# Kernel optimization log

Hardware: AMD Instinct MI355X
Metric: run time of the kernel (lower is better)

Reference implementation:

```python
import jax, jax.numpy as jnp
import numpy as np

DIM = 1024
NUM_HEADS = 16
HEAD_DIM = DIM // NUM_HEADS
B, S = 2, 2048


def setup_inputs() -> dict:
    key = jax.random.key(0)
    k1, k2, k3 = jax.random.split(key, 3)
    x = jax.random.normal(k1, (B, S, DIM), dtype=jnp.float32)
    # torch Linear stores weight [out,in]; we store transposed [in,out] for x @ W
    w_qkv = jax.random.normal(k2, (DIM, 3 * DIM), dtype=jnp.float32) * (DIM ** -0.5)
    b_qkv = jnp.zeros((3 * DIM,), dtype=jnp.float32)
    w_proj = jax.random.normal(k3, (DIM, DIM), dtype=jnp.float32) * (DIM ** -0.5)
    b_proj = jnp.zeros((DIM,), dtype=jnp.float32)
    return {"x": x, "w_qkv": w_qkv, "b_qkv": b_qkv, "w_proj": w_proj, "b_proj": b_proj}


def reference(x, w_qkv, b_qkv, w_proj, b_proj):
    b, s, d = x.shape
    h = HEAD_DIM
    qkv = x @ w_qkv + b_qkv                              # [b,s,3d]
    qkv = qkv.reshape(b, s, 3, NUM_HEADS, h)
    q = jnp.transpose(qkv[:, :, 0], (0, 2, 1, 3))        # [b,nh,s,h]
    k = jnp.transpose(qkv[:, :, 1], (0, 2, 1, 3))
    v = jnp.transpose(qkv[:, :, 2], (0, 2, 1, 3))
    scores = jnp.einsum("bnqh,bnkh->bnqk", q, k) * (h ** -0.5)  # [b,nh,s,s]
    attn = jax.nn.softmax(scores, axis=-1)               # attn_drop is identity (p=0)
    out = jnp.einsum("bnqk,bnkh->bnqh", attn, v)         # [b,nh,s,h]
    out = jnp.transpose(out, (0, 2, 1, 3)).reshape(b, s, d)
    out = out @ w_proj + b_proj                          # proj_drop is identity (p=0)
    return out
```

## Files before the change

### kernel.cpp

```cpp
#include <hip/hip_runtime.h>
#include <hip/hip_bf16.h>

#define DIM    1024
#define NHEADS 16
#define HDIM   64
#define BB     2
#define SS     2048
#define MTOT   (BB * SS)

typedef unsigned short u16;
typedef __attribute__((ext_vector_type(8))) short short8;
typedef __attribute__((ext_vector_type(4))) float f32x4;

__device__ inline u16 f2b(float f) {
  __hip_bfloat16 h = __float2bfloat16(f);
  return *reinterpret_cast<u16*>(&h);
}
__device__ inline f32x4 zero4() { f32x4 v = {0.f, 0.f, 0.f, 0.f}; return v; }

#define GLD_LDS16(GP, LP)                                                   \
  __builtin_amdgcn_global_load_lds(                                         \
      (const __attribute__((address_space(1))) unsigned int*)               \
          (unsigned long long)(const void*)(GP),                            \
      (__attribute__((address_space(3))) unsigned int*)                     \
          (unsigned int)(unsigned long long)(const void*)(LP),              \
      16, 0, 0)

#define QSCALE 0.18033688011112042f

__global__ __launch_bounds__(256) void prep_kernel(
    const float* __restrict__ x, const float* __restrict__ wq,
    const float* __restrict__ wp,
    u16* __restrict__ x_bf, u16* __restrict__ wqt, u16* __restrict__ wpt) {
  __shared__ u16 tile[32][36];
  const int t   = threadIdx.x;
  const int blk = blockIdx.x;
  if (blk < 2048) {
    const int i = blk * 256 + t;
    const float4 a = ((const float4*)x)[i * 2];
    const float4 b = ((const float4*)x)[i * 2 + 1];
    union { u16 u[8]; uint4 v; } r;
    r.u[0] = f2b(a.x); r.u[1] = f2b(a.y); r.u[2] = f2b(a.z); r.u[3] = f2b(a.w);
    r.u[4] = f2b(b.x); r.u[5] = f2b(b.y); r.u[6] = f2b(b.z); r.u[7] = f2b(b.w);
    ((uint4*)x_bf)[i] = r.v;
    return;
  }
  const float* __restrict__ in;
  u16* __restrict__ out;
  int N, n0, k0;
  if (blk < 5120) {
    const int b2 = blk - 2048;
    in = wq; out = wqt; N = 3072;
    n0 = (b2 % 96) * 32; k0 = (b2 / 96) * 32;
  } else {
    const int b2 = blk - 5120;
    in = wp; out = wpt; N = 1024;
    n0 = (b2 & 31) * 32; k0 = (b2 >> 5) * 32;
  }
  const int tr = t >> 3, tc4 = (t & 7) * 4;
  const float4 a = *(const float4*)&in[(size_t)(k0 + tr) * N + n0 + tc4];
  tile[tr][tc4 + 0] = f2b(a.x); tile[tr][tc4 + 1] = f2b(a.y);
  tile[tr][tc4 + 2] = f2b(a.z); tile[tr][tc4 + 3] = f2b(a.w);
  __syncthreads();
  union { u16 u[4]; uint2 v; } pk;
  pk.u[0] = tile[tc4 + 0][tr]; pk.u[1] = tile[tc4 + 1][tr];
  pk.u[2] = tile[tc4 + 2][tr]; pk.u[3] = tile[tc4 + 3][tr];
  *(uint2*)&out[(size_t)(n0 + tr) * DIM + k0 + tc4] = pk.v;
}

__global__ __launch_bounds__(256) void gemm_qkv_bf16(
    const u16* __restrict__ xa, const u16* __restrict__ wt,
    const float* __restrict__ bias,
    u16* __restrict__ qbuf, u16* __restrict__ kbuf, u16* __restrict__ vtbuf) {
  __shared__ __align__(16) u16 As[128 * 64];
  __shared__ __align__(16) u16 Bs[128 * 64];
  const int tid = threadIdx.x, w = tid >> 6, lane = tid & 63;
  const int l15 = lane & 15, l4 = lane >> 4;
  const int lin = blockIdx.x;
  const int swz = (lin & 7) * 96 + (lin >> 3);
  const int m0 = (swz & 31) * 128, n0 = (swz >> 5) * 128;
  const int wm = (w >> 1) * 64, wn = (w & 1) * 64;

  f32x4 acc[4][4];
#pragma unroll
  for (int i = 0; i < 4; ++i)
#pragma unroll
    for (int j = 0; j < 4; ++j) acc[i][j] = zero4();

  for (int k0 = 0; k0 < DIM; k0 += 64) {
#pragma unroll
    for (int j = 0; j < 4; ++j) {
      const int rowX = (w * 4 + j) * 8 + (lane >> 3);
      const int kcol = k0 + (lane & 7) * 8;
      GLD_LDS16(&xa[(size_t)(m0 + rowX) * DIM + kcol], &As[(w * 4 + j) * 512]);
      GLD_LDS16(&wt[(size_t)(n0 + rowX) * DIM + kcol], &Bs[(w * 4 + j) * 512]);
    }
    asm volatile("s_waitcnt vmcnt(0)" ::: "memory");
    __syncthreads();
#pragma unroll
    for (int kc = 0; kc < 2; ++kc) {
      short8 af[4], bfr[4];
#pragma unroll
      for (int mb = 0; mb < 4; ++mb)
        af[mb] = *(const short8*)&As[(wm + mb * 16 + l15) * 64 + kc * 32 + l4 * 8];
#pragma unroll
      for (int nb = 0; nb < 4; ++nb)
        bfr[nb] = *(const short8*)&Bs[(wn + nb * 16 + l15) * 64 + kc * 32 + l4 * 8];
#pragma unroll
      for (int mb = 0; mb < 4; ++mb)
#pragma unroll
        for (int nb = 0; nb < 4; ++nb)
          acc[mb][nb] = __builtin_amdgcn_mfma_f32_16x16x32_bf16(
              af[mb], bfr[nb], acc[mb][nb], 0, 0, 0);
    }
    __syncthreads();
  }

  const int colb  = n0 + wn;
  const int which = colb >> 10;
  const int head  = (colb & 1023) >> 6;
  if (which == 2) {
#pragma unroll
    for (int nb = 0; nb < 4; ++nb) {
      const int col = colb + nb * 16 + l15;
      const float bv = bias[col];
      const int h = col & 63;
#pragma unroll
      for (int mb = 0; mb < 4; ++mb) {
        const int rowbase = m0 + wm + mb * 16 + l4 * 4;
        const int b = rowbase >> 11, s0 = rowbase & 2047;
        union { u16 u[4]; uint2 v; } pk;
#pragma unroll
        for (int r = 0; r < 4; ++r) pk.u[r] = f2b(acc[mb][nb][r] + bv);
        *(uint2*)&vtbuf[((size_t)((b * NHEADS + head) * 64 + h)) * SS + s0] = pk.v;
      }
    }
  } else {
    u16* __restrict__ dst = (which == 0) ? qbuf : kbuf;
    const float scale = (which == 0) ? QSCALE : 1.0f;
#pragma unroll
    for (int nb = 0; nb < 4; ++nb) {
      const int col = colb + nb * 16 + l15;
      const float bv = bias[col];
      const int h = col & 63;
#pragma unroll
      for (int mb = 0; mb < 4; ++mb)
#pragma unroll
        for (int r = 0; r < 4; ++r) {
          const int row = m0 + wm + mb * 16 + l4 * 4 + r;
          const int b = row >> 11, s = row & 2047;
          dst[((size_t)((b * NHEADS + head) * SS + s)) * 64 + h] =
              f2b((acc[mb][nb][r] + bv) * scale);
        }
    }
  }
}

__global__ __launch_bounds__(512, 4) void attn_mfma(
    const u16* __restrict__ qbuf, const u16* __restrict__ kbuf,
    const u16* __restrict__ vtbuf, u16* __restrict__ aobuf) {
  __shared__ __align__(16) u16 Ks[2][64 * 64];
  __shared__ __align__(16) u16 Vs[2][64 * 64];
  __shared__ __align__(16) u16 Ps[8][16 * 64];
  const int tid = threadIdx.x, w = tid >> 6, lane = tid & 63;
  const int l15 = lane & 15, l4 = lane >> 4;
  const int lin = blockIdx.x;
  const int swz = (lin & 7) * 64 + (lin >> 3);
  const int bh = swz >> 4, qt = swz & 15;
  const int b = bh >> 4, head = bh & 15;

  const u16* __restrict__ qsrc  = qbuf + ((size_t)(bh * SS + qt * 128 + w * 16)) * 64;
  const u16* __restrict__ kbase = kbuf + (size_t)bh * SS * 64;
  const u16* __restrict__ vtb   = vtbuf + (size_t)bh * 64 * SS;

  short8 qf[2];
#pragma unroll
  for (int kc = 0; kc < 2; ++kc)
    qf[kc] = *(const short8*)&qsrc[l15 * 64 + kc * 32 + l4 * 8];

  const int srow  = w * 8 + (lane >> 3);
  const int schk  = (lane & 7) ^ (srow & 7);

#define STAGE(t, bi)                                                          \
  {                                                                           \
    GLD_LDS16(kbase + ((size_t)((t) * 64 + srow)) * 64 + schk * 8,            \
              &Ks[bi][w * 8 * 64]);                                           \
    GLD_LDS16(vtb + (size_t)srow * SS + (t) * 64 + schk * 8,                  \
              &Vs[bi][w * 8 * 64]);                                           \
  }

  STAGE(0, 0);
  asm volatile("s_waitcnt vmcnt(0)" ::: "memory");
  __syncthreads();

  f32x4 acco[4];
#pragma unroll
  for (int i = 0; i < 4; ++i) acco[i] = zero4();
  float mrun = -1e30f, lrun = 0.f;

  for (int kt = 0; kt < SS / 64; ++kt) {
    const int cur = kt & 1;

    if (kt + 1 < SS / 64) STAGE(kt + 1, 1 - cur);

    f32x4 sc[4];
#pragma unroll
    for (int i = 0; i < 4; ++i) sc[i] = zero4();
    __builtin_amdgcn_s_setprio(1);
#pragma unroll
    for (int kc = 0; kc < 2; ++kc)
#pragma unroll
      for (int nb = 0; nb < 4; ++nb) {
        const int key = nb * 16 + l15;
        const int cc = (kc * 4 + l4) ^ (l15 & 7);
        const short8 kf = *(const short8*)&Ks[cur][key * 64 + cc * 8];
        sc[nb] = __builtin_amdgcn_mfma_f32_16x16x32_bf16(kf, qf[kc], sc[nb], 0, 0, 0);
      }
    __builtin_amdgcn_s_setprio(0);

    float tmax = sc[0][0];
#pragma unroll
    for (int nb = 0; nb < 4; ++nb)
#pragma unroll
      for (int r = 0; r < 4; ++r) tmax = fmaxf(tmax, sc[nb][r]);
    tmax = fmaxf(tmax, __shfl_xor(tmax, 16));
    tmax = fmaxf(tmax, __shfl_xor(tmax, 32));
    if (__ballot(tmax > mrun + 8.0f)) {
      const float mnew = fmaxf(mrun, tmax);
      const float f = exp2f(mrun - mnew);
      mrun = mnew;
      lrun *= f;
#pragma unroll
      for (int nb = 0; nb < 4; ++nb)
#pragma unroll
        for (int r = 0; r < 4; ++r) acco[nb][r] *= f;
    }
    float p[4][4], rs = 0.f;
#pragma unroll
    for (int nb = 0; nb < 4; ++nb)
#pragma unroll
      for (int r = 0; r < 4; ++r) {
        p[nb][r] = exp2f(sc[nb][r] - mrun);
        rs += p[nb][r];
      }
    rs += __shfl_xor(rs, 16);
    rs += __shfl_xor(rs, 32);
    lrun += rs;

#pragma unroll
    for (int nb = 0; nb < 4; ++nb) {
      union { u16 u[4]; uint2 v; } pk;
#pragma unroll
      for (int r = 0; r < 4; ++r) pk.u[r] = f2b(p[nb][r]);
      const int cc = (nb * 2 + (l4 >> 1)) ^ (l15 & 7);
      *(uint2*)&Ps[w][l15 * 64 + cc * 8 + (l4 & 1) * 4] = pk.v;
    }

    __builtin_amdgcn_s_setprio(1);
#pragma unroll
    for (int kc = 0; kc < 2; ++kc) {
      const int ccp = (kc * 4 + l4) ^ (l15 & 7);
      const short8 pf = *(const short8*)&Ps[w][l15 * 64 + ccp * 8];
#pragma unroll
      for (int nb = 0; nb < 4; ++nb) {
        const int h = nb * 16 + l15;
        const int cv = (kc * 4 + l4) ^ (l15 & 7);
        const short8 vf = *(const short8*)&Vs[cur][h * 64 + cv * 8];
        acco[nb] = __builtin_amdgcn_mfma_f32_16x16x32_bf16(vf, pf, acco[nb], 0, 0, 0);
      }
    }
    __builtin_amdgcn_s_setprio(0);

    asm volatile("s_waitcnt vmcnt(0)" ::: "memory");
    __syncthreads();
  }
#undef STAGE

  const float inv = 1.f / lrun;
  const int s = qt * 128 + w * 16 + l15;
  u16* __restrict__ dst = aobuf + (size_t)(b * SS + s) * DIM + head * 64;
#pragma unroll
  for (int nb = 0; nb < 4; ++nb) {
    union { u16 u[4]; uint2 v; } pk;
#pragma unroll
    for (int r = 0; r < 4; ++r) pk.u[r] = f2b(acco[nb][r] * inv);
    *(uint2*)&dst[nb * 16 + l4 * 4] = pk.v;
  }
}

__global__ __launch_bounds__(256) void gemm_proj_bf16(
    const u16* __restrict__ ao, const u16* __restrict__ wpt,
    const float* __restrict__ bias, float* __restrict__ out) {
  __shared__ __align__(16) u16 As[128 * 64];
  __shared__ __align__(16) u16 Bs[64 * 64];
  const int tid = threadIdx.x, w = tid >> 6, lane = tid & 63;
  const int l15 = lane & 15, l4 = lane >> 4;
  const int lin = blockIdx.x;
  const int swz = (lin & 7) * 64 + (lin >> 3);
  const int m0 = (swz & 31) * 128, n0 = (swz >> 5) * 64;
  const int wm = (w >> 1) * 64, wn = (w & 1) * 32;

  f32x4 acc[4][2];
#pragma unroll
  for (int i = 0; i < 4; ++i)
#pragma unroll
    for (int j = 0; j < 2; ++j) acc[i][j] = zero4();

  for (int k0 = 0; k0 < DIM; k0 += 64) {
#pragma unroll
    for (int j = 0; j < 4; ++j) {
      const int rowA = (w * 4 + j) * 8 + (lane >> 3);
      GLD_LDS16(&ao[(size_t)(m0 + rowA) * DIM + k0 + (lane & 7) * 8],
                &As[(w * 4 + j) * 512]);
    }
#pragma unroll
    for (int j = 0; j < 2; ++j) {
      const int rowB = (w * 2 + j) * 8 + (lane >> 3);
      GLD_LDS16(&wpt[(size_t)(n0 + rowB) * DIM + k0 + (lane & 7) * 8],
                &Bs[(w * 2 + j) * 512]);
    }
    asm volatile("s_waitcnt vmcnt(0)" ::: "memory");
    __syncthreads();
#pragma unroll
    for (int kc = 0; kc < 2; ++kc) {
      short8 af[4], bfr[2];
#pragma unroll
      for (int mb = 0; mb < 4; ++mb)
        af[mb] = *(const short8*)&As[(wm + mb * 16 + l15) * 64 + kc * 32 + l4 * 8];
#pragma unroll
      for (int nb = 0; nb < 2; ++nb)
        bfr[nb] = *(const short8*)&Bs[(wn + nb * 16 + l15) * 64 + kc * 32 + l4 * 8];
#pragma unroll
      for (int mb = 0; mb < 4; ++mb)
#pragma unroll
        for (int nb = 0; nb < 2; ++nb)
          acc[mb][nb] = __builtin_amdgcn_mfma_f32_16x16x32_bf16(
              af[mb], bfr[nb], acc[mb][nb], 0, 0, 0);
    }
    __syncthreads();
  }
#pragma unroll
  for (int nb = 0; nb < 2; ++nb) {
    const int col = n0 + wn + nb * 16 + l15;
    const float bv = bias[col];
#pragma unroll
    for (int mb = 0; mb < 4; ++mb)
#pragma unroll
      for (int r = 0; r < 4; ++r) {
        const int row = m0 + wm + mb * 16 + l4 * 4 + r;
        out[(size_t)row * DIM + col] = acc[mb][nb][r] + bv;
      }
  }
}

extern "C" void kernel_launch(void* const* d_in, const int* in_sizes, int n_in,
                              void* d_out, int out_size, void* d_ws, size_t ws_size,
                              hipStream_t stream) {
  const float* x      = (const float*)d_in[0];
  const float* w_qkv  = (const float*)d_in[1];
  const float* b_qkv  = (const float*)d_in[2];
  const float* w_proj = (const float*)d_in[3];
  const float* b_proj = (const float*)d_in[4];
  float* out = (float*)d_out;

  u16* ws = (u16*)d_ws;
  u16* x_bf    = ws;
  u16* wqkv_t  = x_bf   + (size_t)MTOT * DIM;
  u16* wproj_t = wqkv_t + (size_t)3 * DIM * DIM;
  u16* qbuf    = wproj_t + (size_t)DIM * DIM;
  u16* kbuf    = qbuf + (size_t)MTOT * DIM;
  u16* vtbuf   = kbuf + (size_t)MTOT * DIM;
  u16* aobuf   = vtbuf + (size_t)MTOT * DIM;

  prep_kernel<<<6144, 256, 0, stream>>>(x, w_qkv, w_proj, x_bf, wqkv_t, wproj_t);
  gemm_qkv_bf16<<<768, 256, 0, stream>>>(x_bf, wqkv_t, b_qkv, qbuf, kbuf, vtbuf);
  attn_mfma<<<512, 512, 0, stream>>>(qbuf, kbuf, vtbuf, aobuf);
  gemm_proj_bf16<<<512, 256, 0, stream>>>(aobuf, wproj_t, b_proj, out);
}
```

Baseline: 225.4 us.

## Software-pipeline attention QK^T with softmax/PV and stage V transpose through LDS

The attention loop is restructured so the QK^T MFMAs for the next key tile are issued before the softmax and PV of the current tile. K uses two buffers and V uses three rotating buffers, which overlaps matrix work with the exp/reduction work. The QKV GEMM epilogue for V now writes its transposed tile through shared memory and then stores coalesced 16-byte rows, instead of scattered 8-byte writes. The attention output buffer also reuses the x_bf workspace. The cost is extra LDS, more register pressure from two live score sets, and extra macro complexity.

Result: no change. 223.8 us (-0.7%).

```diff
diff --git a/kernel.cpp b/kernel.cpp
--- a/kernel.cpp
+++ b/kernel.cpp
@@ -120,20 +120,31 @@
   const int which = colb >> 10;
   const int head  = (colb & 1023) >> 6;
   if (which == 2) {
+    u16* __restrict__ wl = ((w < 2) ? As : Bs) + (w & 1) * 4096;
+    const int rowbase = m0 + wm;
+    const int bidx = rowbase >> 11, sbase = rowbase & 2047;
+    float bv[4];
+#pragma unroll
+    for (int nb = 0; nb < 4; ++nb) bv[nb] = bias[colb + nb * 16 + l15];
 #pragma unroll
     for (int nb = 0; nb < 4; ++nb) {
-      const int col = colb + nb * 16 + l15;
-      const float bv = bias[col];
-      const int h = col & 63;
+      const int h = nb * 16 + l15;
 #pragma unroll
       for (int mb = 0; mb < 4; ++mb) {
-        const int rowbase = m0 + wm + mb * 16 + l4 * 4;
-        const int b = rowbase >> 11, s0 = rowbase & 2047;
         union { u16 u[4]; uint2 v; } pk;
 #pragma unroll
-        for (int r = 0; r < 4; ++r) pk.u[r] = f2b(acc[mb][nb][r] + bv);
-        *(uint2*)&vtbuf[((size_t)((b * NHEADS + head) * 64 + h)) * SS + s0] = pk.v;
+        for (int r = 0; r < 4; ++r) pk.u[r] = f2b(acc[mb][nb][r] + bv[nb]);
+        const int csw = (mb * 2 + (l4 >> 1)) ^ (l15 & 7);
+        *(uint2*)&wl[h * 64 + csw * 8 + (l4 & 1) * 4] = pk.v;
       }
+    }
+#pragma unroll
+    for (int p = 0; p < 8; ++p) {
+      const int h = (lane >> 3) + p * 8;
+      const int csw = (lane & 7) ^ (h & 7);
+      const uint4 d = *(const uint4*)&wl[h * 64 + csw * 8];
+      *(uint4*)&vtbuf[((size_t)((bidx * NHEADS + head) * 64 + h)) * SS +
+                      sbase + (lane & 7) * 8] = d;
     }
   } else {
     u16* __restrict__ dst = (which == 0) ? qbuf : kbuf;
@@ -160,7 +171,7 @@
     const u16* __restrict__ qbuf, const u16* __restrict__ kbuf,
     const u16* __restrict__ vtbuf, u16* __restrict__ aobuf) {
   __shared__ __align__(16) u16 Ks[2][64 * 64];
-  __shared__ __align__(16) u16 Vs[2][64 * 64];
+  __shared__ __align__(16) u16 Vs[3 * 64 * 64];
   __shared__ __align__(16) u16 Ps[8][16 * 64];
   const int tid = threadIdx.x, w = tid >> 6, lane = tid & 63;
   const int l15 = lane & 15, l4 = lane >> 4;
@@ -181,15 +192,84 @@
   const int srow  = w * 8 + (lane >> 3);
   const int schk  = (lane & 7) ^ (srow & 7);
 
-#define STAGE(t, bi)                                                          \
+#define STAGEK(t, bi)                                                         \
+  GLD_LDS16(kbase + ((size_t)((t) * 64 + srow)) * 64 + schk * 8,              \
+            &Ks[bi][w * 8 * 64]);
+#define STAGEV(t, vi)                                                         \
+  GLD_LDS16(vtb + (size_t)srow * SS + (t) * 64 + schk * 8,                    \
+            &Vs[(vi) * 4096 + w * 8 * 64]);
+
+#define QKT(KB, sc)                                                           \
   {                                                                           \
-    GLD_LDS16(kbase + ((size_t)((t) * 64 + srow)) * 64 + schk * 8,            \
-              &Ks[bi][w * 8 * 64]);                                           \
-    GLD_LDS16(vtb + (size_t)srow * SS + (t) * 64 + schk * 8,                  \
-              &Vs[bi][w * 8 * 64]);                                           \
-  }
-
-  STAGE(0, 0);
+    _Pragma("unroll") for (int i = 0; i < 4; ++i) sc[i] = zero4();            \
+    __builtin_amdgcn_s_setprio(1);                                            \
+    _Pragma("unroll") for (int kc = 0; kc < 2; ++kc)                          \
+      _Pragma("unroll") for (int nb = 0; nb < 4; ++nb) {                      \
+        const int key = nb * 16 + l15;                                        \
+        const int cc = (kc * 4 + l4) ^ (l15 & 7);                             \
+        const short8 kf = *(const short8*)&(KB)[key * 64 + cc * 8];           \
+        sc[nb] = __builtin_amdgcn_mfma_f32_16x16x32_bf16(kf, qf[kc], sc[nb],  \
+                                                          0, 0, 0);           \
+      }                                                                       \
+    __builtin_amdgcn_s_setprio(0);                                            \
+  }
+
+#define SOFTMAX_P(sc)                                                         \
+  {                                                                           \
+    float t0 = fmaxf(fmaxf(sc[0][0], sc[0][1]), sc[0][2]);                    \
+    t0 = fmaxf(fmaxf(t0, sc[0][3]), sc[1][0]);                                \
+    t0 = fmaxf(fmaxf(t0, sc[1][1]), sc[1][2]);                                \
+    t0 = fmaxf(fmaxf(t0, sc[1][3]), sc[2][0]);                                \
+    t0 = fmaxf(fmaxf(t0, sc[2][1]), sc[2][2]);                                \
+    t0 = fmaxf(fmaxf(t0, sc[2][3]), sc[3][0]);                                \
+    t0 = fmaxf(fmaxf(t0, sc[3][1]), sc[3][2]);                                \
+    float tmax = fmaxf(t0, sc[3][3]);                                         \
+    tmax = fmaxf(tmax, __shfl_xor(tmax, 16));                                 \
+    tmax = fmaxf(tmax, __shfl_xor(tmax, 32));                                 \
+    if (__ballot(tmax > mrun + 8.0f)) {                                       \
+      const float mnew = fmaxf(mrun, tmax);                                   \
+      const float f = exp2f(mrun - mnew);                                     \
+      mrun = mnew;                                                            \
+      lrun *= f;                                                              \
+      _Pragma("unroll") for (int nb = 0; nb < 4; ++nb)                        \
+        _Pragma("unroll") for (int r = 0; r < 4; ++r) acco[nb][r] *= f;       \
+    }                                                                         \
+    float p[4][4], rs = 0.f;                                                  \
+    _Pragma("unroll") for (int nb = 0; nb < 4; ++nb)                          \
+      _Pragma("unroll") for (int r = 0; r < 4; ++r) {                         \
+        p[nb][r] = exp2f(sc[nb][r] - mrun);                                   \
+        rs += p[nb][r];                                                       \
+      }                                                                       \
+    rs += __shfl_xor(rs, 16);                                                 \
+    rs += __shfl_xor(rs, 32);                                                 \
+    lrun += rs;                                                               \
+    _Pragma("unroll") for (int nb = 0; nb < 4; ++nb) {                        \
+      union { u16 u[4]; uint2 v; } pk;                                        \
+      _Pragma("unroll") for (int r = 0; r < 4; ++r) pk.u[r] = f2b(p[nb][r]);  \
+      const int cc = (nb * 2 + (l4 >> 1)) ^ (l15 & 7);                        \
+      *(uint2*)&Ps[w][l15 * 64 + cc * 8 + (l4 & 1) * 4] = pk.v;               \
+    }                                                                         \
+  }
+
+#define PVSTEP(vi)                                                            \
+  {                                                                           \
+    __builtin_amdgcn_s_setprio(1);                                            \
+    _Pragma("unroll") for (int kc = 0; kc < 2; ++kc) {                        \
+      const int ccp = (kc * 4 + l4) ^ (l15 & 7);                              \
+      const short8 pf = *(const short8*)&Ps[w][l15 * 64 + ccp * 8];           \
+      _Pragma("unroll") for (int nb = 0; nb < 4; ++nb) {                      \
+        const int h = nb * 16 + l15;                                          \
+        const int cv = (kc * 4 + l4) ^ (l15 & 7);                             \
+        const short8 vf =                                                     \
+            *(const short8*)&Vs[(vi) * 4096 + h * 64 + cv * 8];               \
+        acco[nb] = __builtin_amdgcn_mfma_f32_16x16x32_bf16(vf, pf, acco[nb],  \
+                                                            0, 0, 0);         \
+      }                                                                       \
+    }                                                                         \
+    __builtin_amdgcn_s_setprio(0);                                            \
+  }
+
+  STAGEK(0, 0); STAGEV(0, 0);
   asm volatile("s_waitcnt vmcnt(0)" ::: "memory");
   __syncthreads();
 
@@ -198,83 +278,38 @@
   for (int i = 0; i < 4; ++i) acco[i] = zero4();
   float mrun = -1e30f, lrun = 0.f;
 
-  for (int kt = 0; kt < SS / 64; ++kt) {
-    const int cur = kt & 1;
-
-    if (kt + 1 < SS / 64) STAGE(kt + 1, 1 - cur);
-
-    f32x4 sc[4];
-#pragma unroll
-    for (int i = 0; i < 4; ++i) sc[i] = zero4();
-    __builtin_amdgcn_s_setprio(1);
-#pragma unroll
-    for (int kc = 0; kc < 2; ++kc)
-#pragma unroll
-      for (int nb = 0; nb < 4; ++nb) {
-        const int key = nb * 16 + l15;
-        const int cc = (kc * 4 + l4) ^ (l15 & 7);
-        const short8 kf = *(const short8*)&Ks[cur][key * 64 + cc * 8];
-        sc[nb] = __builtin_amdgcn_mfma_f32_16x16x32_bf16(kf, qf[kc], sc[nb], 0, 0, 0);
-      }
-    __builtin_amdgcn_s_setprio(0);
-
-    float tmax = sc[0][0];
-#pragma unroll
-    for (int nb = 0; nb < 4; ++nb)
-#pragma unroll
-      for (int r = 0; r < 4; ++r) tmax = fmaxf(tmax, sc[nb][r]);
-    tmax = fmaxf(tmax, __shfl_xor(tmax, 16));
-    tmax = fmaxf(tmax, __shfl_xor(tmax, 32));
-    if (__ballot(tmax > mrun + 8.0f)) {
-      const float mnew = fmaxf(mrun, tmax);
-      const float f = exp2f(mrun - mnew);
-      mrun = mnew;
-      lrun *= f;
-#pragma unroll
-      for (int nb = 0; nb < 4; ++nb)
-#pragma unroll
-        for (int r = 0; r < 4; ++r) acco[nb][r] *= f;
-    }
-    float p[4][4], rs = 0.f;
-#pragma unroll
-    for (int nb = 0; nb < 4; ++nb)
-#pragma unroll
-      for (int r = 0; r < 4; ++r) {
-        p[nb][r] = exp2f(sc[nb][r] - mrun);
-        rs += p[nb][r];
-      }
-    rs += __shfl_xor(rs, 16);
-    rs += __shfl_xor(rs, 32);
-    lrun += rs;
-
-#pragma unroll
-    for (int nb = 0; nb < 4; ++nb) {
-      union { u16 u[4]; uint2 v; } pk;
-#pragma unroll
-      for (int r = 0; r < 4; ++r) pk.u[r] = f2b(p[nb][r]);
-      const int cc = (nb * 2 + (l4 >> 1)) ^ (l15 & 7);
-      *(uint2*)&Ps[w][l15 * 64 + cc * 8 + (l4 & 1) * 4] = pk.v;
-    }
-
-    __builtin_amdgcn_s_setprio(1);
-#pragma unroll
-    for (int kc = 0; kc < 2; ++kc) {
-      const int ccp = (kc * 4 + l4) ^ (l15 & 7);
-      const short8 pf = *(const short8*)&Ps[w][l15 * 64 + ccp * 8];
-#pragma unroll
-      for (int nb = 0; nb < 4; ++nb) {
-        const int h = nb * 16 + l15;
-        const int cv = (kc * 4 + l4) ^ (l15 & 7);
-        const short8 vf = *(const short8*)&Vs[cur][h * 64 + cv * 8];
-        acco[nb] = __builtin_amdgcn_mfma_f32_16x16x32_bf16(vf, pf, acco[nb], 0, 0, 0);
-      }
-    }
-    __builtin_amdgcn_s_setprio(0);
-
+  f32x4 scA[4], scB[4];
+  QKT(Ks[0], scA);
+  STAGEK(1, 1); STAGEV(1, 1);
+
+  int va = 0, vb = 1, vc = 2;
+  for (int t2 = 0; t2 < 16; ++t2) {
+    const int t = 2 * t2;
     asm volatile("s_waitcnt vmcnt(0)" ::: "memory");
     __syncthreads();
-  }
-#undef STAGE
+    QKT(Ks[1], scB);
+    if (t + 2 < 32) { STAGEK(t + 2, 0); STAGEV(t + 2, vc); }
+    SOFTMAX_P(scA);
+    PVSTEP(va);
+    if (t2 < 15) {
+      asm volatile("s_waitcnt vmcnt(0)" ::: "memory");
+      __syncthreads();
+      QKT(Ks[0], scA);
+      STAGEK(t + 3, 1); STAGEV(t + 3, va);
+      SOFTMAX_P(scB);
+      PVSTEP(vb);
+      const int ova = va, ovb = vb;
+      va = vc; vb = ova; vc = ovb;
+    } else {
+      SOFTMAX_P(scB);
+      PVSTEP(vb);
+    }
+  }
+#undef STAGEK
+#undef STAGEV
+#undef QKT
+#undef SOFTMAX_P
+#undef PVSTEP
 
   const float inv = 1.f / lrun;
   const int s = qt * 128 + w * 16 + l15;
@@ -370,7 +405,7 @@
   u16* qbuf    = wproj_t + (size_t)DIM * DIM;
   u16* kbuf    = qbuf + (size_t)MTOT * DIM;
   u16* vtbuf   = kbuf + (size_t)MTOT * DIM;
-  u16* aobuf   = vtbuf + (size_t)MTOT * DIM;
+  u16* aobuf   = x_bf;
 
   prep_kernel<<<6144, 256, 0, stream>>>(x, w_qkv, w_proj, x_bf, wqkv_t, wproj_t);
   gemm_qkv_bf16<<<768, 256, 0, stream>>>(x_bf, wqkv_t, b_qkv, qbuf, kbuf, vtbuf);
```
